# Optimization experiments

Hardware: AMD Instinct MI355X
Metric: run time of the kernel (lower is better)

The kernel has to match this reference:

```python
import jax, jax.numpy as jnp
import numpy as np

B, S, V, D, H, L = 256, 512, 32000, 100, 75, 128

def setup_inputs() -> dict:
    key = jax.random.key(0)
    ks = jax.random.split(key, 10)
    def lin(k, out_f, in_f):
        bound = 1.0 / np.sqrt(in_f)
        kw, kb = jax.random.split(k)
        W = jax.random.uniform(kw, (out_f, in_f), jnp.float32, -bound, bound)
        b = jax.random.uniform(kb, (out_f,), jnp.float32, -bound, bound)
        return W, b
    W1, b1 = lin(ks[0], H, D)   # i2h_fc1
    W2, b2 = lin(ks[1], H, H)   # i2h_fc2
    Wo, bo = lin(ks[2], H, H)   # h2o_fc
    Wfc, bfc = lin(ks[3], L, H) # fc
    emb = jax.random.normal(ks[4], (V, D), jnp.float32)
    X = jax.random.randint(ks[5], (B, S), 0, V)
    return {"X": X, "emb": emb, "W1": W1, "b1": b1, "W2": W2, "b2": b2,
            "Wo": Wo, "bo": bo, "Wfc": Wfc, "bfc": bfc}

def reference(X, emb, W1, b1, W2, b2, Wo, bo, Wfc, bfc):
    x = emb[X]                                   # [B,S,D] embedding lookup (dropout off: is_training=False)
    xp = jnp.einsum('bsd,hd->bsh', x, W1) + b1   # precompute input projection for all steps
    h0 = jnp.zeros((X.shape[0], W2.shape[0]), x.dtype)

    def step(h, xp_t):
        h = jax.nn.sigmoid(xp_t + h @ W2.T + b2)       # Elman hidden update
        o = jax.nn.sigmoid(h @ Wo.T + bo)              # per-step output
        return h, o

    _, outs = jax.lax.scan(step, h0, jnp.swapaxes(xp, 0, 1))  # [S,B,H]
    outs = jnp.swapaxes(outs, 0, 1)                            # [B,S,H] (batch_first)
    return jnp.einsum('bsh,lh->bsl', outs, Wfc) + bfc          # [B,S,L]
```

## Files before the change

### kernel.cpp

```cpp
#include <hip/hip_runtime.h>
#include <hip/hip_bf16.h>

typedef unsigned int uint;
typedef unsigned short ushort;

constexpr int Bn = 256, Sn = 512, Vn = 32000, Dn = 100, Hn = 75, Ln = 128;
constexpr int EW = 80;
constexpr int KP = 96;
constexpr int W2S = 80;

constexpr size_t OFF_EMBW = 0;
constexpr size_t OFF_HALL = OFF_EMBW + (size_t)Vn*EW;
constexpr size_t OFF_W2P  = OFF_HALL + (size_t)Bn*Sn*KP/2;
constexpr size_t OFF_WOH  = OFF_W2P + 3200;
constexpr size_t OFF_WFH  = OFF_WOH + 3840;

typedef __attribute__((ext_vector_type(2))) _Float16 half2_t;
typedef __attribute__((ext_vector_type(8))) _Float16 half8;
typedef __attribute__((ext_vector_type(4))) float floatx4;

__device__ __forceinline__ ushort f2h(float f){
    union { _Float16 h; ushort u; } v; v.h = (_Float16)f; return v.u;
}
__device__ __forceinline__ half8 as_h8(uint4 u){
    union { uint4 u; half8 h; } v; v.u = u; return v.h;
}
__device__ __forceinline__ float sigmoidf(float z){
    return __builtin_amdgcn_rcpf(1.f + __expf(-z));
}

__global__ __launch_bounds__(256) void k_wprep(
    const float* __restrict__ W2, const float* __restrict__ Wo,
    const float* __restrict__ Wfc, ushort* __restrict__ w2p,
    ushort* __restrict__ woh, ushort* __restrict__ wfh, ushort* __restrict__ h_all)
{
    const int tid = blockIdx.x*256 + threadIdx.x;
    const int stride = gridDim.x*256;
    for (int i = tid; i < 80*W2S; i += stride){
        int r = i / W2S, k = i % W2S;
        w2p[i] = (r < Hn && k < Hn) ? f2h(W2[r*Hn + k]) : (ushort)0;
    }
    for (int i = tid; i < 80*KP; i += stride){
        int r = i / KP, k = i % KP;
        woh[i] = (r < Hn && k < Hn) ? f2h(Wo[r*Hn + k]) : (ushort)0;
    }
    for (int i = tid; i < Ln*KP; i += stride){
        int l = i / KP, k = i % KP;
        wfh[i] = (k < Hn) ? f2h(Wfc[l*Hn + k]) : (ushort)0;
    }
    uint* hu = (uint*)h_all;
    for (int i = tid; i < Bn*Sn*8; i += stride){
        int row = i >> 3, c = i & 7;
        hu[(size_t)row*48 + 40 + c] = 0u;
    }
}

__global__ __attribute__((amdgpu_flat_work_group_size(64,64)))
__attribute__((amdgpu_waves_per_eu(1,1)))
void k_embproj(
    const float* __restrict__ emb, const float* __restrict__ W1,
    const float* __restrict__ b1, const float* __restrict__ b2,
    float* __restrict__ embW)
{
    const int lane = threadIdx.x;
    const int v = blockIdx.x*64 + lane;
    const float4* ev = (const float4*)(emb + (size_t)v*Dn);
    float e[Dn];
    #pragma unroll
    for (int q = 0; q < Dn/4; ++q){
        float4 x = ev[q];
        e[4*q] = x.x; e[4*q+1] = x.y; e[4*q+2] = x.z; e[4*q+3] = x.w;
    }
    __shared__ float s_out[64*EW];
    #pragma unroll 4
    for (int j = 0; j < Hn; ++j){
        float a0 = b1[j] + b2[j], a1 = 0.f, a2 = 0.f, a3 = 0.f;
        const float* w = W1 + j*Dn;
        #pragma unroll
        for (int d = 0; d < Dn; d += 4){
            a0 += w[d]*e[d];     a1 += w[d+1]*e[d+1];
            a2 += w[d+2]*e[d+2]; a3 += w[d+3]*e[d+3];
        }
        s_out[lane*EW + j] = (a0+a1) + (a2+a3);
    }
    #pragma unroll
    for (int j = Hn; j < EW; ++j) s_out[lane*EW + j] = 0.f;
    __syncthreads();
    float* dst = embW + (size_t)blockIdx.x*64*EW;
    for (int i = lane; i < 64*EW; i += 64) dst[i] = s_out[i];
}

__global__ __attribute__((amdgpu_flat_work_group_size(64,64)))
__attribute__((amdgpu_waves_per_eu(1,1)))
void k_rnn(
    const int* __restrict__ X, const float* __restrict__ embW,
    const ushort* __restrict__ w2p, ushort* __restrict__ h_all)
{
    const int b = blockIdx.x;
    const int L = threadIdx.x;
    const int m = L & 15;
    const int g = L >> 4;
    __shared__ int sX[Sn];

    for (int i = L; i < Sn; i += 64) sX[i] = X[b*Sn + i];

    half8 bfr[5][3];
    #pragma unroll
    for (int t = 0; t < 5; ++t){
        #pragma unroll
        for (int ks = 0; ks < 3; ++ks){
            int k0 = ks*32 + g*8;
            half8 bv = {};
            if (k0 < 80) bv = *(const half8*)(w2p + (size_t)(16*t + m)*W2S + k0);
            bfr[t][ks] = bv;
        }
    }
    __syncthreads();

    int va0 = 32*g,      va1 = 32*g + 8,  va2 = 32*g + 16, va3 = 32*g + 24;
    int vb0 = va0 + 128, vb1 = va1 + 128, vb2 = va2 + 128, vb3 = va3 + 128;

    ushort* hout = h_all + (size_t)b*Sn*KP;
    float x1c, x2c, x1n, x2n, x1m, x2m;
    {
        int t0 = sX[0], t1 = sX[1], t2 = sX[2];
        x1c = embW[(size_t)t0*EW + L];
        x2c = (L < 16) ? embW[(size_t)t0*EW + 64 + L] : 0.f;
        x1n = embW[(size_t)t1*EW + L];
        x2n = (L < 16) ? embW[(size_t)t1*EW + 64 + L] : 0.f;
        x1m = embW[(size_t)t2*EW + L];
        x2m = (L < 16) ? embW[(size_t)t2*EW + 64 + L] : 0.f;
    }
    const floatx4 zero4 = {};
    uint4 A0 = {}, A1 = {}, A2 = {};

    for (int s = 0; s < Sn; ++s){
        int tok = sX[(s+3 < Sn) ? s+3 : Sn-1];
        float x1f = embW[(size_t)tok*EW + L];
        float x2f = (L < 16) ? embW[(size_t)tok*EW + 64 + L] : 0.f;

        half8 af0 = as_h8(A0), af1 = as_h8(A1), af2 = as_h8(A2);

        floatx4 acc0, acc1, acc2, acc3, acc4;
        acc0 = __builtin_amdgcn_mfma_f32_16x16x32_f16(af0, bfr[0][0], zero4, 0,0,0);
        acc1 = __builtin_amdgcn_mfma_f32_16x16x32_f16(af0, bfr[1][0], zero4, 0,0,0);
        acc2 = __builtin_amdgcn_mfma_f32_16x16x32_f16(af0, bfr[2][0], zero4, 0,0,0);
        acc3 = __builtin_amdgcn_mfma_f32_16x16x32_f16(af0, bfr[3][0], zero4, 0,0,0);
        acc4 = __builtin_amdgcn_mfma_f32_16x16x32_f16(af0, bfr[4][0], zero4, 0,0,0);
        acc0 = __builtin_amdgcn_mfma_f32_16x16x32_f16(af1, bfr[0][1], acc0, 0,0,0);
        acc1 = __builtin_amdgcn_mfma_f32_16x16x32_f16(af1, bfr[1][1], acc1, 0,0,0);
        acc2 = __builtin_amdgcn_mfma_f32_16x16x32_f16(af1, bfr[2][1], acc2, 0,0,0);
        acc3 = __builtin_amdgcn_mfma_f32_16x16x32_f16(af1, bfr[3][1], acc3, 0,0,0);
        acc4 = __builtin_amdgcn_mfma_f32_16x16x32_f16(af1, bfr[4][1], acc4, 0,0,0);
        acc0 = __builtin_amdgcn_mfma_f32_16x16x32_f16(af2, bfr[0][2], acc0, 0,0,0);
        acc1 = __builtin_amdgcn_mfma_f32_16x16x32_f16(af2, bfr[1][2], acc1, 0,0,0);
        acc2 = __builtin_amdgcn_mfma_f32_16x16x32_f16(af2, bfr[2][2], acc2, 0,0,0);
        acc3 = __builtin_amdgcn_mfma_f32_16x16x32_f16(af2, bfr[3][2], acc3, 0,0,0);
        acc4 = __builtin_amdgcn_mfma_f32_16x16x32_f16(af2, bfr[4][2], acc4, 0,0,0);

        float y1 = (L < 32) ? ((L < 16) ? acc0[0] : acc1[0])
                            : ((L < 48) ? acc2[0] : acc3[0]);
        float y2 = acc4[0];

        float h1 = sigmoidf(y1 + x1c);
        float h2 = sigmoidf(y2 + x2c);
        if (L >= 11) h2 = 0.f;
        ushort u1 = f2h(h1);
        ushort u2 = f2h(h2);
        hout[(size_t)s*KP + L] = u1;
        if (L < 16) hout[(size_t)s*KP + 64 + L] = u2;

        uint v1 = u1, v2 = u2;
        uint pr1 = (uint)__builtin_amdgcn_update_dpp(0, (int)v1, 0xB1, 0xF, 0xF, true);
        uint pr2 = (uint)__builtin_amdgcn_update_dpp(0, (int)v2, 0xB1, 0xF, 0xF, true);
        int q1 = (int)(v1 | (pr1 << 16));
        int q2 = (int)(v2 | (pr2 << 16));

        A0.x = (uint)__builtin_amdgcn_ds_bpermute(va0, q1);
        A0.y = (uint)__builtin_amdgcn_ds_bpermute(va1, q1);
        A0.z = (uint)__builtin_amdgcn_ds_bpermute(va2, q1);
        A0.w = (uint)__builtin_amdgcn_ds_bpermute(va3, q1);
        A1.x = (uint)__builtin_amdgcn_ds_bpermute(vb0, q1);
        A1.y = (uint)__builtin_amdgcn_ds_bpermute(vb1, q1);
        A1.z = (uint)__builtin_amdgcn_ds_bpermute(vb2, q1);
        A1.w = (uint)__builtin_amdgcn_ds_bpermute(vb3, q1);
        A2.x = (uint)__builtin_amdgcn_ds_bpermute(va0, q2);
        A2.y = (uint)__builtin_amdgcn_ds_bpermute(va1, q2);
        A2.z = (uint)__builtin_amdgcn_ds_bpermute(va2, q2);
        A2.w = (uint)__builtin_amdgcn_ds_bpermute(va3, q2);

        x1c = x1n; x2c = x2n; x1n = x1m; x2n = x2m; x1m = x1f; x2m = x2f;
    }
}

__global__ __launch_bounds__(256) void k_out(
    const ushort* __restrict__ h_all, const ushort* __restrict__ woh,
    const ushort* __restrict__ wfh, const float* __restrict__ bo,
    const float* __restrict__ bfc, float* __restrict__ out)
{
    const int lane = threadIdx.x & 63;
    const int w    = threadIdx.x >> 6;
    const size_t r0 = (size_t)blockIdx.x*64 + w*16;
    const int m = lane & 15;
    const int g = lane >> 4;
    __shared__ __align__(16) ushort o_lds[4][16*104];
    ushort* ot = o_lds[w];
    for (int i = lane; i < 128; i += 64){
        int row = i >> 3, cw = i & 7;
        *(uint*)&ot[row*104 + 80 + cw*2] = 0u;
    }
    floatx4 acc1[5] = {};
    const ushort* hbase = h_all + r0*KP;
    #pragma unroll
    for (int ks = 0; ks < 3; ++ks){
        half8 a = *(const half8*)(hbase + (size_t)m*KP + ks*32 + g*8);
        #pragma unroll
        for (int t = 0; t < 5; ++t){
            half8 bt = *(const half8*)(woh + (16*t + m)*KP + ks*32 + g*8);
            acc1[t] = __builtin_amdgcn_mfma_f32_16x16x32_f16(a, bt, acc1[t], 0, 0, 0);
        }
    }
    #pragma unroll
    for (int t = 0; t < 5; ++t){
        int n = 16*t + m;
        float bias = (n < Hn) ? bo[n] : 0.f;
        #pragma unroll
        for (int r = 0; r < 4; ++r){
            int row = g*4 + r;
            float o = 1.f/(1.f + __expf(-(acc1[t][r] + bias)));
            if (n >= Hn) o = 0.f;
            ot[row*104 + n] = f2h(o);
        }
    }
    floatx4 acc2[8] = {};
    #pragma unroll
    for (int ks = 0; ks < 3; ++ks){
        half8 a = *(const half8*)(ot + m*104 + ks*32 + g*8);
        #pragma unroll
        for (int t = 0; t < 8; ++t){
            half8 bt = *(const half8*)(wfh + (16*t + m)*KP + ks*32 + g*8);
            acc2[t] = __builtin_amdgcn_mfma_f32_16x16x32_f16(a, bt, acc2[t], 0, 0, 0);
        }
    }
    float* orow = out + r0*Ln;
    #pragma unroll
    for (int t = 0; t < 8; ++t){
        float bias = bfc[16*t + m];
        #pragma unroll
        for (int r = 0; r < 4; ++r){
            int row = g*4 + r;
            orow[(size_t)row*Ln + 16*t + m] = acc2[t][r] + bias;
        }
    }
}

extern "C" void kernel_launch(void* const* d_in, const int* in_sizes, int n_in,
                              void* d_out, int out_size, void* d_ws, size_t ws_size,
                              hipStream_t stream)
{
    const int*   X   = (const int*)d_in[0];
    const float* emb = (const float*)d_in[1];
    const float* W1  = (const float*)d_in[2];
    const float* b1  = (const float*)d_in[3];
    const float* W2  = (const float*)d_in[4];
    const float* b2  = (const float*)d_in[5];
    const float* Wo  = (const float*)d_in[6];
    const float* bo  = (const float*)d_in[7];
    const float* Wfc = (const float*)d_in[8];
    const float* bfc = (const float*)d_in[9];
    float* out = (float*)d_out;
    float* ws  = (float*)d_ws;

    float*  embW = ws + OFF_EMBW;
    ushort* hall = (ushort*)(ws + OFF_HALL);
    ushort* w2p  = (ushort*)(ws + OFF_W2P);
    ushort* woh  = (ushort*)(ws + OFF_WOH);
    ushort* wfh  = (ushort*)(ws + OFF_WFH);

    k_wprep<<<dim3(512), dim3(256), 0, stream>>>(W2, Wo, Wfc, w2p, woh, wfh, hall);
    k_embproj<<<dim3(Vn/64), dim3(64), 0, stream>>>(emb, W1, b1, b2, embW);
    k_rnn<<<dim3(Bn), dim3(64), 0, stream>>>(X, embW, w2p, hall);
    k_out<<<dim3((Bn*Sn)/64), dim3(256), 0, stream>>>(hall, woh, wfh, bo, bfc, out);
}
```

Before: 367.6 us.

## Stage projected-embedding rows into double-buffered LDS via async global_load_lds

The recurrent kernel no longer issues a dependent global gather of the projected embedding row every step. It now bulk-copies 64 steps' worth of rows into a double-buffered LDS tile with global_load_lds, prefetching the next chunk while the current one is consumed. Per-step reads then come from LDS, which keeps global-memory latency off the serial recurrence critical path. The cost is 40KB of LDS plus a block barrier every 64 steps, and the async loads have no explicit wait beyond __syncthreads.

```diff
diff --git a/kernel.cpp b/kernel.cpp
--- a/kernel.cpp
+++ b/kernel.cpp
@@ -101,6 +101,7 @@
     const int m = L & 15;
     const int g = L >> 4;
     __shared__ int sX[Sn];
+    __shared__ __align__(16) float xpb[2][64*80];
 
     for (int i = L; i < Sn; i += 64) sX[i] = X[b*Sn + i];
 
@@ -117,79 +118,97 @@
     }
     __syncthreads();
 
+    auto stage = [&](int c){
+        float* buf = xpb[c & 1];
+        const int base = c*64;
+        #pragma unroll
+        for (int k = 0; k < 20; ++k){
+            int idx = k*64 + L;
+            int cs  = idx / 20;
+            int off = idx - cs*20;
+            int tok = sX[base + cs];
+            const float* src = embW + (size_t)tok*EW + off*4;
+            __builtin_amdgcn_global_load_lds(
+                (const __attribute__((address_space(1))) uint*)src,
+                (__attribute__((address_space(3))) uint*)(buf + k*256),
+                16, 0, 0);
+        }
+    };
+
     int va0 = 32*g,      va1 = 32*g + 8,  va2 = 32*g + 16, va3 = 32*g + 24;
     int vb0 = va0 + 128, vb1 = va1 + 128, vb2 = va2 + 128, vb3 = va3 + 128;
 
     ushort* hout = h_all + (size_t)b*Sn*KP;
-    float x1c, x2c, x1n, x2n, x1m, x2m;
-    {
-        int t0 = sX[0], t1 = sX[1], t2 = sX[2];
-        x1c = embW[(size_t)t0*EW + L];
-        x2c = (L < 16) ? embW[(size_t)t0*EW + 64 + L] : 0.f;
-        x1n = embW[(size_t)t1*EW + L];
-        x2n = (L < 16) ? embW[(size_t)t1*EW + 64 + L] : 0.f;
-        x1m = embW[(size_t)t2*EW + L];
-        x2m = (L < 16) ? embW[(size_t)t2*EW + 64 + L] : 0.f;
-    }
     const floatx4 zero4 = {};
     uint4 A0 = {}, A1 = {}, A2 = {};
 
-    for (int s = 0; s < Sn; ++s){
-        int tok = sX[(s+3 < Sn) ? s+3 : Sn-1];
-        float x1f = embW[(size_t)tok*EW + L];
-        float x2f = (L < 16) ? embW[(size_t)tok*EW + 64 + L] : 0.f;
-
-        half8 af0 = as_h8(A0), af1 = as_h8(A1), af2 = as_h8(A2);
-
-        floatx4 acc0, acc1, acc2, acc3, acc4;
-        acc0 = __builtin_amdgcn_mfma_f32_16x16x32_f16(af0, bfr[0][0], zero4, 0,0,0);
-        acc1 = __builtin_amdgcn_mfma_f32_16x16x32_f16(af0, bfr[1][0], zero4, 0,0,0);
-        acc2 = __builtin_amdgcn_mfma_f32_16x16x32_f16(af0, bfr[2][0], zero4, 0,0,0);
-        acc3 = __builtin_amdgcn_mfma_f32_16x16x32_f16(af0, bfr[3][0], zero4, 0,0,0);
-        acc4 = __builtin_amdgcn_mfma_f32_16x16x32_f16(af0, bfr[4][0], zero4, 0,0,0);
-        acc0 = __builtin_amdgcn_mfma_f32_16x16x32_f16(af1, bfr[0][1], acc0, 0,0,0);
-        acc1 = __builtin_amdgcn_mfma_f32_16x16x32_f16(af1, bfr[1][1], acc1, 0,0,0);
-        acc2 = __builtin_amdgcn_mfma_f32_16x16x32_f16(af1, bfr[2][1], acc2, 0,0,0);
-        acc3 = __builtin_amdgcn_mfma_f32_16x16x32_f16(af1, bfr[3][1], acc3, 0,0,0);
-        acc4 = __builtin_amdgcn_mfma_f32_16x16x32_f16(af1, bfr[4][1], acc4, 0,0,0);
-        acc0 = __builtin_amdgcn_mfma_f32_16x16x32_f16(af2, bfr[0][2], acc0, 0,0,0);
-        acc1 = __builtin_amdgcn_mfma_f32_16x16x32_f16(af2, bfr[1][2], acc1, 0,0,0);
-        acc2 = __builtin_amdgcn_mfma_f32_16x16x32_f16(af2, bfr[2][2], acc2, 0,0,0);
-        acc3 = __builtin_amdgcn_mfma_f32_16x16x32_f16(af2, bfr[3][2], acc3, 0,0,0);
-        acc4 = __builtin_amdgcn_mfma_f32_16x16x32_f16(af2, bfr[4][2], acc4, 0,0,0);
-
-        float y1 = (L < 32) ? ((L < 16) ? acc0[0] : acc1[0])
-                            : ((L < 48) ? acc2[0] : acc3[0]);
-        float y2 = acc4[0];
-
-        float h1 = sigmoidf(y1 + x1c);
-        float h2 = sigmoidf(y2 + x2c);
-        if (L >= 11) h2 = 0.f;
-        ushort u1 = f2h(h1);
-        ushort u2 = f2h(h2);
-        hout[(size_t)s*KP + L] = u1;
-        if (L < 16) hout[(size_t)s*KP + 64 + L] = u2;
-
-        uint v1 = u1, v2 = u2;
-        uint pr1 = (uint)__builtin_amdgcn_update_dpp(0, (int)v1, 0xB1, 0xF, 0xF, true);
-        uint pr2 = (uint)__builtin_amdgcn_update_dpp(0, (int)v2, 0xB1, 0xF, 0xF, true);
-        int q1 = (int)(v1 | (pr1 << 16));
-        int q2 = (int)(v2 | (pr2 << 16));
-
-        A0.x = (uint)__builtin_amdgcn_ds_bpermute(va0, q1);
-        A0.y = (uint)__builtin_amdgcn_ds_bpermute(va1, q1);
-        A0.z = (uint)__builtin_amdgcn_ds_bpermute(va2, q1);
-        A0.w = (uint)__builtin_amdgcn_ds_bpermute(va3, q1);
-        A1.x = (uint)__builtin_amdgcn_ds_bpermute(vb0, q1);
-        A1.y = (uint)__builtin_amdgcn_ds_bpermute(vb1, q1);
-        A1.z = (uint)__builtin_amdgcn_ds_bpermute(vb2, q1);
-        A1.w = (uint)__builtin_amdgcn_ds_bpermute(vb3, q1);
-        A2.x = (uint)__builtin_amdgcn_ds_bpermute(va0, q2);
-        A2.y = (uint)__builtin_amdgcn_ds_bpermute(va1, q2);
-        A2.z = (uint)__builtin_amdgcn_ds_bpermute(va2, q2);
-        A2.w = (uint)__builtin_amdgcn_ds_bpermute(va3, q2);
-
-        x1c = x1n; x2c = x2n; x1n = x1m; x2n = x2m; x1m = x1f; x2m = x2f;
+    stage(0);
+    for (int c = 0; c < 8; ++c){
+        __syncthreads();
+        if (c < 7) stage(c + 1);
+        const float* xp = xpb[c & 1];
+        float x1c = xp[L];
+        float x2c = (L < 16) ? xp[64 + L] : 0.f;
+        float x1n = xp[80 + L];
+        float x2n = (L < 16) ? xp[80 + 64 + L] : 0.f;
+        for (int t = 0; t < 64; ++t){
+            int pf = (t + 2 < 64) ? t + 2 : 63;
+            float x1f = xp[pf*80 + L];
+            float x2f = (L < 16) ? xp[pf*80 + 64 + L] : 0.f;
+
+            half8 af0 = as_h8(A0), af1 = as_h8(A1), af2 = as_h8(A2);
+
+            floatx4 acc0, acc1, acc2, acc3, acc4;
+            acc0 = __builtin_amdgcn_mfma_f32_16x16x32_f16(af0, bfr[0][0], zero4, 0,0,0);
+            acc1 = __builtin_amdgcn_mfma_f32_16x16x32_f16(af0, bfr[1][0], zero4, 0,0,0);
+            acc2 = __builtin_amdgcn_mfma_f32_16x16x32_f16(af0, bfr[2][0], zero4, 0,0,0);
+            acc3 = __builtin_amdgcn_mfma_f32_16x16x32_f16(af0, bfr[3][0], zero4, 0,0,0);
+            acc4 = __builtin_amdgcn_mfma_f32_16x16x32_f16(af0, bfr[4][0], zero4, 0,0,0);
+            acc0 = __builtin_amdgcn_mfma_f32_16x16x32_f16(af1, bfr[0][1], acc0, 0,0,0);
+            acc1 = __builtin_amdgcn_mfma_f32_16x16x32_f16(af1, bfr[1][1], acc1, 0,0,0);
+            acc2 = __builtin_amdgcn_mfma_f32_16x16x32_f16(af1, bfr[2][1], acc2, 0,0,0);
+            acc3 = __builtin_amdgcn_mfma_f32_16x16x32_f16(af1, bfr[3][1], acc3, 0,0,0);
+            acc4 = __builtin_amdgcn_mfma_f32_16x16x32_f16(af1, bfr[4][1], acc4, 0,0,0);
+            acc0 = __builtin_amdgcn_mfma_f32_16x16x32_f16(af2, bfr[0][2], acc0, 0,0,0);
+            acc1 = __builtin_amdgcn_mfma_f32_16x16x32_f16(af2, bfr[1][2], acc1, 0,0,0);
+            acc2 = __builtin_amdgcn_mfma_f32_16x16x32_f16(af2, bfr[2][2], acc2, 0,0,0);
+            acc3 = __builtin_amdgcn_mfma_f32_16x16x32_f16(af2, bfr[3][2], acc3, 0,0,0);
+            acc4 = __builtin_amdgcn_mfma_f32_16x16x32_f16(af2, bfr[4][2], acc4, 0,0,0);
+
+            float y1 = (L < 32) ? ((L < 16) ? acc0[0] : acc1[0])
+                                : ((L < 48) ? acc2[0] : acc3[0]);
+            float y2 = acc4[0];
+
+            float h1 = sigmoidf(y1 + x1c);
+            float h2 = sigmoidf(y2 + x2c);
+            if (L >= 11) h2 = 0.f;
+            ushort u1 = f2h(h1);
+            ushort u2 = f2h(h2);
+            int s = c*64 + t;
+            hout[(size_t)s*KP + L] = u1;
+            if (L < 16) hout[(size_t)s*KP + 64 + L] = u2;
+
+            uint v1 = u1, v2 = u2;
+            uint pr1 = (uint)__builtin_amdgcn_update_dpp(0, (int)v1, 0xB1, 0xF, 0xF, true);
+            uint pr2 = (uint)__builtin_amdgcn_update_dpp(0, (int)v2, 0xB1, 0xF, 0xF, true);
+            int q1 = (int)(v1 | (pr1 << 16));
+            int q2 = (int)(v2 | (pr2 << 16));
+
+            A0.x = (uint)__builtin_amdgcn_ds_bpermute(va0, q1);
+            A0.y = (uint)__builtin_amdgcn_ds_bpermute(va1, q1);
+            A0.z = (uint)__builtin_amdgcn_ds_bpermute(va2, q1);
+            A0.w = (uint)__builtin_amdgcn_ds_bpermute(va3, q1);
+            A1.x = (uint)__builtin_amdgcn_ds_bpermute(vb0, q1);
+            A1.y = (uint)__builtin_amdgcn_ds_bpermute(vb1, q1);
+            A1.z = (uint)__builtin_amdgcn_ds_bpermute(vb2, q1);
+            A1.w = (uint)__builtin_amdgcn_ds_bpermute(vb3, q1);
+            A2.x = (uint)__builtin_amdgcn_ds_bpermute(va0, q2);
+            A2.y = (uint)__builtin_amdgcn_ds_bpermute(va1, q2);
+            A2.z = (uint)__builtin_amdgcn_ds_bpermute(va2, q2);
+            A2.w = (uint)__builtin_amdgcn_ds_bpermute(va3, q2);
+
+            x1c = x1n; x2c = x2n; x1n = x1f; x2n = x2f;
+        }
     }
 }
 
```

New measurement: 352.8 us. 4.0% less time.
